# Performance work log

Measured on AMD Instinct MI355X. Metric: run time of the kernel, lower is better.

## Reference

```python
import jax, jax.numpy as jnp
import numpy as np

NUM_KERNELS = 64
KERNEL_DIM = 16

def setup_inputs() -> dict:
    key = jax.random.key(0)
    kx, kt = jax.random.split(key)
    B, F = 512, 1024
    x = jax.random.normal(kx, (B, F), dtype=jnp.float32)
    # xavier_uniform for T: limit = sqrt(6/(fan_in+fan_out))
    fan_in, fan_out = F, NUM_KERNELS * KERNEL_DIM
    limit = float(np.sqrt(6.0 / (fan_in + fan_out)))
    T = jax.random.uniform(kt, (F, fan_out), dtype=jnp.float32, minval=-limit, maxval=limit)
    return {"x": x, "T": T}

def reference(x, T):
    B = x.shape[0]
    M = (x @ T).reshape(B, NUM_KERNELS, KERNEL_DIM)          # [B, K, D]
    # all-pairs L1 distance over D: [B, B, K]
    l1 = jnp.abs(M[None, :, :, :] - M[:, None, :, :]).sum(axis=3)
    Kmat = jnp.exp(-l1)                                        # [B, B, K]
    return Kmat.sum(axis=1) - 1.0                              # [B, K]
```

## Files before the change

kernel.cpp:

```cpp
#include <hip/hip_runtime.h>
#include <hip/hip_fp16.h>

#define BB 512
#define FF 1024
#define NK 64
#define KD 16

typedef __attribute__((ext_vector_type(4))) float f32x4;
typedef __attribute__((ext_vector_type(8))) _Float16 half8;

__device__ __forceinline__ unsigned short f16_bits(float f) {
    __half h = __float2half(f);
    return *reinterpret_cast<unsigned short*>(&h);
}

__global__ __launch_bounds__(256) void md_prep_kernel(
    const float* __restrict__ x, const float* __restrict__ T,
    unsigned short* __restrict__ xf, unsigned short* __restrict__ Tf) {
    const int b = blockIdx.x;
    const int t = threadIdx.x;
    if (b < 256) {
        __shared__ float tile[64][65];
        const int k0 = (b >> 4) * 64, n0 = (b & 15) * 64;
        #pragma unroll
        for (int rr = 0; rr < 4; ++rr) {
            const int kk = rr * 16 + (t >> 4);
            const float4 v = *(const float4*)&T[(size_t)(k0 + kk) * FF + n0 + (t & 15) * 4];
            tile[kk][(t & 15) * 4 + 0] = v.x; tile[kk][(t & 15) * 4 + 1] = v.y;
            tile[kk][(t & 15) * 4 + 2] = v.z; tile[kk][(t & 15) * 4 + 3] = v.w;
        }
        __syncthreads();
        #pragma unroll
        for (int rr = 0; rr < 4; ++rr) {
            const int nl = rr * 16 + (t >> 4);
            const int kl = (t & 15) * 4;
            ushort4 h;
            h.x = f16_bits(tile[kl + 0][nl]);
            h.y = f16_bits(tile[kl + 1][nl]);
            h.z = f16_bits(tile[kl + 2][nl]);
            h.w = f16_bits(tile[kl + 3][nl]);
            *(ushort4*)&Tf[(size_t)(n0 + nl) * FF + k0 + kl] = h;
        }
    } else {
        const int base = (b - 256) * 256 + t;
        #pragma unroll
        for (int s = 0; s < 4; ++s) {
            const int idx = s * 32768 + base;
            const float4 v = *(const float4*)&x[(size_t)idx * 4];
            ushort4 h;
            h.x = f16_bits(v.x); h.y = f16_bits(v.y);
            h.z = f16_bits(v.z); h.w = f16_bits(v.w);
            *(ushort4*)&xf[(size_t)idx * 4] = h;
        }
    }
}

__global__ __launch_bounds__(512) void md_mfma_kernel(
    const unsigned short* __restrict__ xf, const unsigned short* __restrict__ Tf,
    float* __restrict__ M2, float* __restrict__ out) {
    __shared__ __align__(16) unsigned short lds[2][6144];

    const int t = threadIdx.x, w = t >> 6, l = t & 63;
    const int b = blockIdx.x, xc = b & 7, s = b >> 3;
    const int mt = (xc & 1) * 8 + (s & 7);
    const int nt = (xc >> 1) * 4 + (s >> 3);

    if (b < 2) {
        const float4 z = make_float4(0.f, 0.f, 0.f, 0.f);
        #pragma unroll
        for (int q = 0; q < 8; ++q)
            *(float4*)&out[(size_t)(b * 4096 + q * 512 + t) * 4] = z;
    }

    const int col16s = (l & 7) ^ (l >> 3);
    const unsigned short* gA = xf + ((size_t)mt * 32 + (w & 3) * 8 + (l >> 3)) * FF + col16s * 8;
    const unsigned short* gB = Tf + ((size_t)nt * 64 + w * 8 + (l >> 3)) * FF + col16s * 8;
    const int ldsA = (w & 3) * 8 * 64;
    const int ldsB = 2048 + w * 8 * 64;

    const int lrow = l & 15, lkg = l >> 4;
    const int ar = (w >> 2) * 16 + lrow;
    const int br = (w & 3) * 16 + lrow;
    const int swa = ar & 7, swb = br & 7;

    f32x4 acc = {};

    if (w < 4)
        __builtin_amdgcn_global_load_lds(
            (const __attribute__((address_space(1))) void*)gA,
            (__attribute__((address_space(3))) void*)&lds[0][ldsA], 16, 0, 0);
    __builtin_amdgcn_global_load_lds(
        (const __attribute__((address_space(1))) void*)gB,
        (__attribute__((address_space(3))) void*)&lds[0][ldsB], 16, 0, 0);
    __syncthreads();

    int buf = 0;
    for (int it = 0; it < 16; ++it) {
        if (it < 15) {
            const int kt = (it + 1) * 64;
            if (w < 4)
                __builtin_amdgcn_global_load_lds(
                    (const __attribute__((address_space(1))) void*)(gA + kt),
                    (__attribute__((address_space(3))) void*)&lds[buf ^ 1][ldsA], 16, 0, 0);
            __builtin_amdgcn_global_load_lds(
                (const __attribute__((address_space(1))) void*)(gB + kt),
                (__attribute__((address_space(3))) void*)&lds[buf ^ 1][ldsB], 16, 0, 0);
        }
        const unsigned short* L = lds[buf];
        #pragma unroll
        for (int ks = 0; ks < 2; ++ks) {
            const int cb = ks * 4 + lkg;
            const half8 a = *(const half8*)&L[ar * 64 + (cb ^ swa) * 8];
            const half8 v = *(const half8*)&L[2048 + br * 64 + (cb ^ swb) * 8];
            acc = __builtin_amdgcn_mfma_f32_16x16x32_f16(a, v, acc, 0, 0, 0);
        }
        __syncthreads();
        buf ^= 1;
    }

    const int kblk = nt * 4 + (w & 3);
    const int rowb = mt * 32 + (w >> 2) * 16 + lkg * 4;
    #pragma unroll
    for (int rg = 0; rg < 4; ++rg)
        M2[((size_t)kblk * BB + rowb + rg) * KD + lrow] = acc[rg];
}

__global__ __launch_bounds__(256) void md_pairwise_sym_kernel(
    const float* __restrict__ M2, float* __restrict__ out) {
    __shared__ float Mi[64][20];
    __shared__ float Mj[64][16];
    __shared__ float et[64][65];
    __shared__ float part_row[4][64];
    __shared__ float part_col[4][64];

    const int bx = blockIdx.x;
    const int k = bx & 63;
    int p = bx >> 6;
    int it = 0;
    while (p >= 8 - it) { p -= 8 - it; ++it; }
    const int jt = it + p;
    const bool diag = (it == jt);
    const int t = threadIdx.x;

    const float* tileI = M2 + ((size_t)k * BB + it * 64) * KD;
    const float* tileJ = M2 + ((size_t)k * BB + jt * 64) * KD;
    {
        const int row = t >> 2, dg = (t & 3) * 4;
        const float4 a = *(const float4*)&tileI[t * 4];
        *(float4*)&Mi[row][dg] = a;
        const float4 c = *(const float4*)&tileJ[t * 4];
        *(float4*)&Mj[row][dg] = c;
    }
    __syncthreads();

    const int i = t & 63;
    const int wv = t >> 6;

    float mi[16];
    #pragma unroll
    for (int dg = 0; dg < 4; ++dg) {
        const float4 v = *(const float4*)&Mi[i][dg * 4];
        mi[dg * 4 + 0] = v.x; mi[dg * 4 + 1] = v.y;
        mi[dg * 4 + 2] = v.z; mi[dg * 4 + 3] = v.w;
    }

    float row_acc = 0.0f;
    #pragma unroll 4
    for (int jj = 0; jj < 16; ++jj) {
        const int j = wv * 16 + jj;
        const float4* mj = (const float4*)&Mj[j][0];
        const float4 v0 = mj[0], v1 = mj[1], v2 = mj[2], v3 = mj[3];
        float p0 = (fabsf(mi[0] - v0.x) + fabsf(mi[1] - v0.y)) +
                   (fabsf(mi[2] - v0.z) + fabsf(mi[3] - v0.w));
        float p1 = (fabsf(mi[4] - v1.x) + fabsf(mi[5] - v1.y)) +
                   (fabsf(mi[6] - v1.z) + fabsf(mi[7] - v1.w));
        float p2 = (fabsf(mi[8] - v2.x) + fabsf(mi[9] - v2.y)) +
                   (fabsf(mi[10] - v2.z) + fabsf(mi[11] - v2.w));
        float p3 = (fabsf(mi[12] - v3.x) + fabsf(mi[13] - v3.y)) +
                   (fabsf(mi[14] - v3.z) + fabsf(mi[15] - v3.w));
        const float e = __expf(-((p0 + p1) + (p2 + p3)));
        row_acc += e;
        et[i][j] = e;
    }
    part_row[wv][i] = row_acc;
    __syncthreads();

    if (!diag) {
        const int j = t & 63;
        const int chunk = t >> 6;
        float col_acc = 0.0f;
        #pragma unroll
        for (int ii = 0; ii < 16; ++ii)
            col_acc += et[chunk * 16 + ii][j];
        part_col[chunk][j] = col_acc;
    }
    __syncthreads();

    if (t < 64) {
        float r = ((part_row[0][t] + part_row[1][t]) +
                   (part_row[2][t] + part_row[3][t])) - (diag ? 1.0f : 0.0f);
        atomicAdd(&out[(size_t)(it * 64 + t) * NK + k], r);
    } else if (t < 128 && !diag) {
        const int j = t - 64;
        float c = (part_col[0][j] + part_col[1][j]) +
                  (part_col[2][j] + part_col[3][j]);
        atomicAdd(&out[(size_t)(jt * 64 + j) * NK + k], c);
    }
}

extern "C" void kernel_launch(void* const* d_in, const int* in_sizes, int n_in,
                              void* d_out, int out_size, void* d_ws, size_t ws_size,
                              hipStream_t stream) {
    const float* x = (const float*)d_in[0];
    const float* T = (const float*)d_in[1];
    float* out = (float*)d_out;

    unsigned short* xf = (unsigned short*)d_ws;
    unsigned short* Tf = xf + (size_t)BB * FF;
    float* M2 = (float*)(Tf + (size_t)FF * FF);

    md_prep_kernel<<<384, 256, 0, stream>>>(x, T, xf, Tf);
    md_mfma_kernel<<<dim3(256), 512, 0, stream>>>(xf, Tf, M2, out);
    md_pairwise_sym_kernel<<<dim3(36 * 64), 256, 0, stream>>>(M2, out);
}
```

Baseline: 35.50 us.

## Fuse GEMM and pairwise kernels with a grid-wide atomic barrier

Merges the MFMA projection kernel and the pairwise L1/exp kernel into one persistent 256-block launch. The two phases share LDS through a union and are separated by a software grid barrier (atomic counter plus spin). Each block then handles 9 pairwise tiles using 512 threads, and the GEMM tile mapping and the T transpose block ordering are remapped for locality. This removes one launch and its tail, but the spin barrier relies on all 256 blocks being co-resident, and each block works through its pairwise tiles one after another.

```diff
diff --git a/kernel.cpp b/kernel.cpp
--- a/kernel.cpp
+++ b/kernel.cpp
@@ -16,12 +16,14 @@
 
 __global__ __launch_bounds__(256) void md_prep_kernel(
     const float* __restrict__ x, const float* __restrict__ T,
-    unsigned short* __restrict__ xf, unsigned short* __restrict__ Tf) {
+    unsigned short* __restrict__ xf, unsigned short* __restrict__ Tf,
+    int* __restrict__ bar) {
     const int b = blockIdx.x;
     const int t = threadIdx.x;
     if (b < 256) {
         __shared__ float tile[64][65];
-        const int k0 = (b >> 4) * 64, n0 = (b & 15) * 64;
+        const int n0 = (2 * (b & 7) + ((b >> 3) & 1)) * 64;
+        const int k0 = (b >> 4) * 64;
         #pragma unroll
         for (int rr = 0; rr < 4; ++rr) {
             const int kk = rr * 16 + (t >> 4);
@@ -42,6 +44,7 @@
             *(ushort4*)&Tf[(size_t)(n0 + nl) * FF + k0 + kl] = h;
         }
     } else {
+        if (b == 256 && t == 0) *bar = 0;
         const int base = (b - 256) * 256 + t;
         #pragma unroll
         for (int s = 0; s < 4; ++s) {
@@ -55,156 +58,175 @@
     }
 }
 
-__global__ __launch_bounds__(512) void md_mfma_kernel(
+__global__ __launch_bounds__(512) void md_gemm_pair_kernel(
     const unsigned short* __restrict__ xf, const unsigned short* __restrict__ Tf,
-    float* __restrict__ M2, float* __restrict__ out) {
-    __shared__ __align__(16) unsigned short lds[2][6144];
+    float* __restrict__ M2, float* __restrict__ out, int* __restrict__ bar) {
+    union Sh {
+        unsigned short glds[2][6144];
+        struct {
+            float Mi[64][20];
+            float Mj[64][16];
+            float et[64][65];
+            float pr[8][64];
+            float pc[8][64];
+        } pw;
+    };
+    __shared__ Sh sh;
 
     const int t = threadIdx.x, w = t >> 6, l = t & 63;
     const int b = blockIdx.x, xc = b & 7, s = b >> 3;
-    const int mt = (xc & 1) * 8 + (s & 7);
-    const int nt = (xc >> 1) * 4 + (s >> 3);
-
-    if (b < 2) {
-        const float4 z = make_float4(0.f, 0.f, 0.f, 0.f);
-        #pragma unroll
-        for (int q = 0; q < 8; ++q)
-            *(float4*)&out[(size_t)(b * 4096 + q * 512 + t) * 4] = z;
-    }
-
-    const int col16s = (l & 7) ^ (l >> 3);
-    const unsigned short* gA = xf + ((size_t)mt * 32 + (w & 3) * 8 + (l >> 3)) * FF + col16s * 8;
-    const unsigned short* gB = Tf + ((size_t)nt * 64 + w * 8 + (l >> 3)) * FF + col16s * 8;
-    const int ldsA = (w & 3) * 8 * 64;
-    const int ldsB = 2048 + w * 8 * 64;
-
-    const int lrow = l & 15, lkg = l >> 4;
-    const int ar = (w >> 2) * 16 + lrow;
-    const int br = (w & 3) * 16 + lrow;
-    const int swa = ar & 7, swb = br & 7;
-
-    f32x4 acc = {};
-
-    if (w < 4)
+
+    {
+        const int nt = xc * 2 + (s & 1);
+        const int mt = s >> 1;
+
+        if (b < 2) {
+            const float4 z = make_float4(0.f, 0.f, 0.f, 0.f);
+            #pragma unroll
+            for (int q = 0; q < 8; ++q)
+                *(float4*)&out[(size_t)(b * 4096 + q * 512 + t) * 4] = z;
+        }
+
+        const int col16s = (l & 7) ^ (l >> 3);
+        const unsigned short* gA = xf + ((size_t)mt * 32 + (w & 3) * 8 + (l >> 3)) * FF + col16s * 8;
+        const unsigned short* gB = Tf + ((size_t)nt * 64 + w * 8 + (l >> 3)) * FF + col16s * 8;
+        const int ldsA = (w & 3) * 8 * 64;
+        const int ldsB = 2048 + w * 8 * 64;
+
+        const int lrow = l & 15, lkg = l >> 4;
+        const int ar = (w >> 2) * 16 + lrow;
+        const int br = (w & 3) * 16 + lrow;
+        const int swa = ar & 7, swb = br & 7;
+
+        f32x4 acc = {};
+
+        if (w < 4)
+            __builtin_amdgcn_global_load_lds(
+                (const __attribute__((address_space(1))) void*)gA,
+                (__attribute__((address_space(3))) void*)&sh.glds[0][ldsA], 16, 0, 0);
         __builtin_amdgcn_global_load_lds(
-            (const __attribute__((address_space(1))) void*)gA,
-            (__attribute__((address_space(3))) void*)&lds[0][ldsA], 16, 0, 0);
-    __builtin_amdgcn_global_load_lds(
-        (const __attribute__((address_space(1))) void*)gB,
-        (__attribute__((address_space(3))) void*)&lds[0][ldsB], 16, 0, 0);
+            (const __attribute__((address_space(1))) void*)gB,
+            (__attribute__((address_space(3))) void*)&sh.glds[0][ldsB], 16, 0, 0);
+        __syncthreads();
+
+        int buf = 0;
+        for (int it = 0; it < 16; ++it) {
+            if (it < 15) {
+                const int kt = (it + 1) * 64;
+                if (w < 4)
+                    __builtin_amdgcn_global_load_lds(
+                        (const __attribute__((address_space(1))) void*)(gA + kt),
+                        (__attribute__((address_space(3))) void*)&sh.glds[buf ^ 1][ldsA], 16, 0, 0);
+                __builtin_amdgcn_global_load_lds(
+                    (const __attribute__((address_space(1))) void*)(gB + kt),
+                    (__attribute__((address_space(3))) void*)&sh.glds[buf ^ 1][ldsB], 16, 0, 0);
+            }
+            const unsigned short* L = sh.glds[buf];
+            #pragma unroll
+            for (int ks = 0; ks < 2; ++ks) {
+                const int cb = ks * 4 + lkg;
+                const half8 a = *(const half8*)&L[ar * 64 + (cb ^ swa) * 8];
+                const half8 v = *(const half8*)&L[2048 + br * 64 + (cb ^ swb) * 8];
+                acc = __builtin_amdgcn_mfma_f32_16x16x32_f16(a, v, acc, 0, 0, 0);
+            }
+            __syncthreads();
+            buf ^= 1;
+        }
+
+        const int kblk = nt * 4 + (w & 3);
+        const int rowb = mt * 32 + (w >> 2) * 16 + lkg * 4;
+        #pragma unroll
+        for (int rg = 0; rg < 4; ++rg)
+            M2[((size_t)kblk * BB + rowb + rg) * KD + lrow] = acc[rg];
+    }
+
+    __threadfence();
     __syncthreads();
-
-    int buf = 0;
-    for (int it = 0; it < 16; ++it) {
-        if (it < 15) {
-            const int kt = (it + 1) * 64;
-            if (w < 4)
-                __builtin_amdgcn_global_load_lds(
-                    (const __attribute__((address_space(1))) void*)(gA + kt),
-                    (__attribute__((address_space(3))) void*)&lds[buf ^ 1][ldsA], 16, 0, 0);
-            __builtin_amdgcn_global_load_lds(
-                (const __attribute__((address_space(1))) void*)(gB + kt),
-                (__attribute__((address_space(3))) void*)&lds[buf ^ 1][ldsB], 16, 0, 0);
-        }
-        const unsigned short* L = lds[buf];
-        #pragma unroll
-        for (int ks = 0; ks < 2; ++ks) {
-            const int cb = ks * 4 + lkg;
-            const half8 a = *(const half8*)&L[ar * 64 + (cb ^ swa) * 8];
-            const half8 v = *(const half8*)&L[2048 + br * 64 + (cb ^ swb) * 8];
-            acc = __builtin_amdgcn_mfma_f32_16x16x32_f16(a, v, acc, 0, 0, 0);
-        }
-        __syncthreads();
-        buf ^= 1;
-    }
-
-    const int kblk = nt * 4 + (w & 3);
-    const int rowb = mt * 32 + (w >> 2) * 16 + lkg * 4;
-    #pragma unroll
-    for (int rg = 0; rg < 4; ++rg)
-        M2[((size_t)kblk * BB + rowb + rg) * KD + lrow] = acc[rg];
-}
-
-__global__ __launch_bounds__(256) void md_pairwise_sym_kernel(
-    const float* __restrict__ M2, float* __restrict__ out) {
-    __shared__ float Mi[64][20];
-    __shared__ float Mj[64][16];
-    __shared__ float et[64][65];
-    __shared__ float part_row[4][64];
-    __shared__ float part_col[4][64];
-
-    const int bx = blockIdx.x;
-    const int k = bx & 63;
-    int p = bx >> 6;
-    int it = 0;
-    while (p >= 8 - it) { p -= 8 - it; ++it; }
-    const int jt = it + p;
-    const bool diag = (it == jt);
-    const int t = threadIdx.x;
-
-    const float* tileI = M2 + ((size_t)k * BB + it * 64) * KD;
-    const float* tileJ = M2 + ((size_t)k * BB + jt * 64) * KD;
-    {
-        const int row = t >> 2, dg = (t & 3) * 4;
-        const float4 a = *(const float4*)&tileI[t * 4];
-        *(float4*)&Mi[row][dg] = a;
-        const float4 c = *(const float4*)&tileJ[t * 4];
-        *(float4*)&Mj[row][dg] = c;
+    if (t == 0) {
+        atomicAdd(bar, 1);
+        while (__hip_atomic_load(bar, __ATOMIC_RELAXED, __HIP_MEMORY_SCOPE_AGENT) < 256)
+            __builtin_amdgcn_s_sleep(8);
     }
     __syncthreads();
-
-    const int i = t & 63;
-    const int wv = t >> 6;
-
-    float mi[16];
-    #pragma unroll
-    for (int dg = 0; dg < 4; ++dg) {
-        const float4 v = *(const float4*)&Mi[i][dg * 4];
-        mi[dg * 4 + 0] = v.x; mi[dg * 4 + 1] = v.y;
-        mi[dg * 4 + 2] = v.z; mi[dg * 4 + 3] = v.w;
-    }
-
-    float row_acc = 0.0f;
-    #pragma unroll 4
-    for (int jj = 0; jj < 16; ++jj) {
-        const int j = wv * 16 + jj;
-        const float4* mj = (const float4*)&Mj[j][0];
-        const float4 v0 = mj[0], v1 = mj[1], v2 = mj[2], v3 = mj[3];
-        float p0 = (fabsf(mi[0] - v0.x) + fabsf(mi[1] - v0.y)) +
-                   (fabsf(mi[2] - v0.z) + fabsf(mi[3] - v0.w));
-        float p1 = (fabsf(mi[4] - v1.x) + fabsf(mi[5] - v1.y)) +
-                   (fabsf(mi[6] - v1.z) + fabsf(mi[7] - v1.w));
-        float p2 = (fabsf(mi[8] - v2.x) + fabsf(mi[9] - v2.y)) +
-                   (fabsf(mi[10] - v2.z) + fabsf(mi[11] - v2.w));
-        float p3 = (fabsf(mi[12] - v3.x) + fabsf(mi[13] - v3.y)) +
-                   (fabsf(mi[14] - v3.z) + fabsf(mi[15] - v3.w));
-        const float e = __expf(-((p0 + p1) + (p2 + p3)));
-        row_acc += e;
-        et[i][j] = e;
-    }
-    part_row[wv][i] = row_acc;
-    __syncthreads();
-
-    if (!diag) {
-        const int j = t & 63;
-        const int chunk = t >> 6;
-        float col_acc = 0.0f;
-        #pragma unroll
-        for (int ii = 0; ii < 16; ++ii)
-            col_acc += et[chunk * 16 + ii][j];
-        part_col[chunk][j] = col_acc;
-    }
-    __syncthreads();
-
-    if (t < 64) {
-        float r = ((part_row[0][t] + part_row[1][t]) +
-                   (part_row[2][t] + part_row[3][t])) - (diag ? 1.0f : 0.0f);
-        atomicAdd(&out[(size_t)(it * 64 + t) * NK + k], r);
-    } else if (t < 128 && !diag) {
-        const int j = t - 64;
-        float c = (part_col[0][j] + part_col[1][j]) +
-                  (part_col[2][j] + part_col[3][j]);
-        atomicAdd(&out[(size_t)(jt * 64 + j) * NK + k], c);
+    __threadfence();
+
+    const int cu = b >> 3;
+    for (int u = 0; u < 9; ++u) {
+        const int beta = cu * 9 + u;
+        const int k = 8 * xc + (beta & 7);
+        int p = beta >> 3;
+        int it = 0;
+        while (p >= 8 - it) { p -= 8 - it; ++it; }
+        const int jt = it + p;
+        const bool diag = (it == jt);
+
+        __syncthreads();
+        {
+            const int tt = t & 255;
+            const int row = tt >> 2, dg = (tt & 3) * 4;
+            const float* tile = (t < 256)
+                ? M2 + ((size_t)k * BB + it * 64) * KD
+                : M2 + ((size_t)k * BB + jt * 64) * KD;
+            const float4 a = *(const float4*)&tile[tt * 4];
+            if (t < 256) *(float4*)&sh.pw.Mi[row][dg] = a;
+            else         *(float4*)&sh.pw.Mj[row][dg] = a;
+        }
+        __syncthreads();
+
+        const int i = t & 63;
+        const int wv = t >> 6;
+
+        float mi[16];
+        #pragma unroll
+        for (int dg = 0; dg < 4; ++dg) {
+            const float4 v = *(const float4*)&sh.pw.Mi[i][dg * 4];
+            mi[dg * 4 + 0] = v.x; mi[dg * 4 + 1] = v.y;
+            mi[dg * 4 + 2] = v.z; mi[dg * 4 + 3] = v.w;
+        }
+
+        float row_acc = 0.0f;
+        #pragma unroll
+        for (int jj = 0; jj < 8; ++jj) {
+            const int j = wv * 8 + jj;
+            const float4* mj = (const float4*)&sh.pw.Mj[j][0];
+            const float4 v0 = mj[0], v1 = mj[1], v2 = mj[2], v3 = mj[3];
+            float p0 = (fabsf(mi[0] - v0.x) + fabsf(mi[1] - v0.y)) +
+                       (fabsf(mi[2] - v0.z) + fabsf(mi[3] - v0.w));
+            float p1 = (fabsf(mi[4] - v1.x) + fabsf(mi[5] - v1.y)) +
+                       (fabsf(mi[6] - v1.z) + fabsf(mi[7] - v1.w));
+            float p2 = (fabsf(mi[8] - v2.x) + fabsf(mi[9] - v2.y)) +
+                       (fabsf(mi[10] - v2.z) + fabsf(mi[11] - v2.w));
+            float p3 = (fabsf(mi[12] - v3.x) + fabsf(mi[13] - v3.y)) +
+                       (fabsf(mi[14] - v3.z) + fabsf(mi[15] - v3.w));
+            const float e = __expf(-((p0 + p1) + (p2 + p3)));
+            row_acc += e;
+            sh.pw.et[i][j] = e;
+        }
+        sh.pw.pr[wv][i] = row_acc;
+        __syncthreads();
+
+        if (!diag) {
+            const int j = t & 63;
+            const int chunk = t >> 6;
+            float col_acc = 0.0f;
+            #pragma unroll
+            for (int ii = 0; ii < 8; ++ii)
+                col_acc += sh.pw.et[chunk * 8 + ii][j];
+            sh.pw.pc[chunk][j] = col_acc;
+        }
+        __syncthreads();
+
+        if (t < 64) {
+            float r = ((sh.pw.pr[0][t] + sh.pw.pr[1][t]) + (sh.pw.pr[2][t] + sh.pw.pr[3][t])) +
+                      ((sh.pw.pr[4][t] + sh.pw.pr[5][t]) + (sh.pw.pr[6][t] + sh.pw.pr[7][t])) -
+                      (diag ? 1.0f : 0.0f);
+            atomicAdd(&out[(size_t)(it * 64 + t) * NK + k], r);
+        } else if (t < 128 && !diag) {
+            const int j = t - 64;
+            float c = ((sh.pw.pc[0][j] + sh.pw.pc[1][j]) + (sh.pw.pc[2][j] + sh.pw.pc[3][j])) +
+                      ((sh.pw.pc[4][j] + sh.pw.pc[5][j]) + (sh.pw.pc[6][j] + sh.pw.pc[7][j]));
+            atomicAdd(&out[(size_t)(jt * 64 + j) * NK + k], c);
+        }
     }
 }
 
@@ -218,8 +240,8 @@
     unsigned short* xf = (unsigned short*)d_ws;
     unsigned short* Tf = xf + (size_t)BB * FF;
     float* M2 = (float*)(Tf + (size_t)FF * FF);
-
-    md_prep_kernel<<<384, 256, 0, stream>>>(x, T, xf, Tf);
-    md_mfma_kernel<<<dim3(256), 512, 0, stream>>>(xf, Tf, M2, out);
-    md_pairwise_sym_kernel<<<dim3(36 * 64), 256, 0, stream>>>(M2, out);
-}
+    int* bar = (int*)(M2 + (size_t)NK * BB * KD);
+
+    md_prep_kernel<<<384, 256, 0, stream>>>(x, T, xf, Tf, bar);
+    md_gemm_pair_kernel<<<dim3(256), 512, 0, stream>>>(xf, Tf, M2, out, bar);
+}
```

Result: slower. 120.9 us (+240.7%).
